# Kernel tuning notes

Measured on AMD Instinct MI355X. Metric: run time of the kernel, lower is better.

The kernel has to match this reference:

```python
import jax, jax.numpy as jnp
import numpy as np

N_NODES = 100000
N_EDGES = 1600000
IN_C, HID_C, OUT_C = 128, 128, 40


def setup_inputs() -> dict:
    key = jax.random.key(0)
    ks = jax.random.split(key, 10)
    def lin(k, fin, fout):
        return jax.random.normal(k, (fin, fout), jnp.float32) / np.sqrt(fin).astype(np.float32)
    return {
        "x": jax.random.normal(ks[0], (N_NODES, IN_C), jnp.float32),
        "edge_index": jax.random.randint(ks[1], (2, N_EDGES), 0, N_NODES, jnp.int64),
        "W1a": lin(ks[2], IN_C, HID_C), "b1a": jnp.zeros((HID_C,), jnp.float32),
        "W1b": lin(ks[3], HID_C, HID_C), "b1b": jnp.zeros((HID_C,), jnp.float32),
        "W2a": lin(ks[4], HID_C, HID_C), "b2a": jnp.zeros((HID_C,), jnp.float32),
        "W2b": lin(ks[5], HID_C, OUT_C), "b2b": jnp.zeros((OUT_C,), jnp.float32),
    }


def gin_conv(x, edge_index, Wa, ba, Wb, bb):
    # GINConv with eps=0: h_i = MLP(x_i + sum_{j in N(i)} x_j)
    src, dst = edge_index[0], edge_index[1]
    agg = jax.ops.segment_sum(x[src], dst, num_segments=N_NODES)  # [N, C]
    h = x + agg
    h = jnp.maximum(h @ Wa + ba, 0.0)  # Linear + ReLU
    return h @ Wb + bb                 # Linear


def reference(x, edge_index, W1a, b1a, W1b, b1b, W2a, b2a, W2b, b2b):
    h = gin_conv(x, edge_index, W1a, b1a, W1b, b1b)
    h = jnp.maximum(h, 0.0)
    # dropout(p=0.5) treated as identity (eval mode / deterministic reference)
    h = gin_conv(h, edge_index, W2a, b2a, W2b, b2b)
    return jax.nn.log_softmax(h, axis=1)
```

## Files before the change

kernel.cpp:

```cpp
#include <hip/hip_runtime.h>

#define N_NODES 100000
#define N_EDGES 1600000
#define CH 128
#define OUTC 40
#define CAP 64
#define NBKT 98
#define BKT_CAP 18432
#define P1_EDGES 4096
#define ROW4 16
#define QROW2 16
#define QSCALE (6.5f / 127.0f)
#define QINV   (127.0f / 6.5f)

typedef __attribute__((ext_vector_type(8))) short bf16x8s;
typedef __attribute__((ext_vector_type(4))) float f32x4;

__device__ __forceinline__ unsigned short f2b_rne(float f) {
    union { float f; unsigned int u; } c; c.f = f;
    unsigned int r = (c.u + 0x7FFF + ((c.u >> 16) & 1)) >> 16;
    return (unsigned short)r;
}
__device__ __forceinline__ float b2f(unsigned short b) {
    union { float f; unsigned int u; } c; c.u = ((unsigned int)b) << 16;
    return c.f;
}
__device__ __forceinline__ int q8(float f) {
    return __float2int_rn(fminf(fmaxf(f * QINV, -127.f), 127.f));
}
__device__ __forceinline__ void addq4(int* a, unsigned int v) {
    a[0] += (int)(v << 24) >> 24;
    a[1] += (int)(v << 16) >> 24;
    a[2] += (int)(v << 8) >> 24;
    a[3] += (int)v >> 24;
}

__global__ __launch_bounds__(256) void conv_f32_bf16_i8(const float4* __restrict__ in,
                                                        ushort4* __restrict__ outb,
                                                        uint2* __restrict__ outq, int n8) {
    int i = blockIdx.x * 256 + threadIdx.x;
    if (i >= n8) return;
    float4 a = in[i * 2], b = in[i * 2 + 1];
    ushort4 o0, o1;
    o0.x = f2b_rne(a.x); o0.y = f2b_rne(a.y); o0.z = f2b_rne(a.z); o0.w = f2b_rne(a.w);
    o1.x = f2b_rne(b.x); o1.y = f2b_rne(b.y); o1.z = f2b_rne(b.z); o1.w = f2b_rne(b.w);
    outb[i * 2] = o0; outb[i * 2 + 1] = o1;
    uint2 q;
    q.x = (unsigned)(q8(a.x) & 0xFF) | ((unsigned)(q8(a.y) & 0xFF) << 8) |
          ((unsigned)(q8(a.z) & 0xFF) << 16) | ((unsigned)(q8(a.w) & 0xFF) << 24);
    q.y = (unsigned)(q8(b.x) & 0xFF) | ((unsigned)(q8(b.y) & 0xFF) << 8) |
          ((unsigned)(q8(b.z) & 0xFF) << 16) | ((unsigned)(q8(b.w) & 0xFF) << 24);
    outq[i] = q;
}

__global__ __launch_bounds__(256) void zero_ints(int* __restrict__ p, int n) {
    int i = blockIdx.x * 256 + threadIdx.x;
    if (i < n) p[i] = 0;
}

__global__ __launch_bounds__(256) void bin_edges(const int* __restrict__ esrc,
                                                 const int* __restrict__ edst,
                                                 int* __restrict__ gcursor,
                                                 unsigned int* __restrict__ bins) {
    __shared__ uint2 stage[P1_EDGES];
    __shared__ int lcnt[NBKT];
    __shared__ int lofs[NBKT];
    __shared__ int lpos[NBKT];
    __shared__ int gbase[NBKT];
    const int tid = threadIdx.x;
    const int e0 = blockIdx.x * P1_EDGES;

    for (int i = tid; i < NBKT; i += 256) lcnt[i] = 0;
    __syncthreads();

    int s[16], d[16];
#pragma unroll
    for (int i = 0; i < 16; ++i) {
        int e = e0 + i * 256 + tid;
        if (e < N_EDGES) { s[i] = esrc[e]; d[i] = edst[e]; }
        else d[i] = -1;
    }
#pragma unroll
    for (int i = 0; i < 16; ++i)
        if (d[i] >= 0) atomicAdd(&lcnt[d[i] >> 10], 1);
    __syncthreads();

    if (tid < NBKT) lofs[tid] = lcnt[tid];
    __syncthreads();
    for (int dd = 1; dd < NBKT; dd <<= 1) {
        int v = 0;
        if (tid < NBKT && tid >= dd) v = lofs[tid - dd];
        __syncthreads();
        if (tid < NBKT) lofs[tid] += v;
        __syncthreads();
    }
    if (tid < NBKT) {
        lpos[tid] = lofs[tid] - lcnt[tid];
        gbase[tid] = atomicAdd(&gcursor[tid], lcnt[tid]);
    }
    __syncthreads();

#pragma unroll
    for (int i = 0; i < 16; ++i) {
        if (d[i] >= 0) {
            int b = d[i] >> 10;
            int slot = atomicAdd(&lpos[b], 1);
            stage[slot] = make_uint2((unsigned)s[i], (unsigned)d[i]);
        }
    }
    __syncthreads();

    int total = lofs[NBKT - 1];
    for (int r = tid; r < total; r += 256) {
        uint2 rec = stage[r];
        int b = (int)(rec.y >> 10);
        int excl = lofs[b] - lcnt[b];
        int pos = gbase[b] + (r - excl);
        unsigned p = ((rec.y & 1023u) << 17) | rec.x;
        if (pos < BKT_CAP) bins[(size_t)b * BKT_CAP + pos] = p;
    }
}

__global__ __launch_bounds__(256) void build_from_bins(const unsigned int* __restrict__ bins,
                                                       const int* __restrict__ gcursor,
                                                       int* __restrict__ adj,
                                                       int* __restrict__ cnt) {
    __shared__ int lc[1024];
    const int b = blockIdx.x;
    const int tid = threadIdx.x;
    const int base = b << 10;
    for (int i = tid; i < 1024; i += 256) lc[i] = 0;
    __syncthreads();
    int n = gcursor[b]; if (n > BKT_CAP) n = BKT_CAP;
    const unsigned int* myb = bins + (size_t)b * BKT_CAP;
    for (int i = tid; i < n; i += 256) {
        unsigned p = myb[i];
        int local = (int)(p >> 17);
        int src = (int)(p & 0x1FFFFu);
        int slot = atomicAdd(&lc[local], 1);
        if (slot < CAP) adj[((base + local) << 6) + slot] = src;
    }
    __syncthreads();
    for (int i = tid; i < 1024; i += 256) {
        int node = base + i;
        if (node < N_NODES) cnt[node] = lc[i];
    }
}

__global__ __launch_bounds__(256) void pack_w3(const float* __restrict__ W0,
                                               const float* __restrict__ W1,
                                               const float* __restrict__ W2,
                                               unsigned short* __restrict__ P0,
                                               unsigned short* __restrict__ P1,
                                               unsigned short* __restrict__ P2) {
    int t = blockIdx.x * 256 + threadIdx.x;
    if (t >= 3 * 2048) return;
    int which = t >> 11;
    int rem = t & 2047;
    int lane = rem & 63;
    int ks = (rem >> 6) & 3;
    int nt = rem >> 8;
    const float* W = which == 0 ? W0 : (which == 1 ? W1 : W2);
    unsigned short* P = which == 0 ? P0 : (which == 1 ? P1 : P2);
    int n = nt * 16 + (lane & 15);
    int kbase = ks * 32 + (lane >> 4) * 8;
    unsigned short* dst = P + ((nt * 4 + ks) * 64 + lane) * 8;
#pragma unroll
    for (int j = 0; j < 8; ++j)
        dst[j] = f2b_rne(W[(kbase + j) * CH + n]);
}

__global__ __launch_bounds__(256) void pack_wout(const float* __restrict__ W,
                                                 unsigned short* __restrict__ P) {
    int t = blockIdx.x * 256 + threadIdx.x;
    if (t >= 768) return;
    int nt = t >> 8, rem = t & 255;
    int ks = rem >> 6, lane = rem & 63;
    int n = nt * 16 + (lane & 15);
    int kbase = ks * 32 + (lane >> 4) * 8;
    unsigned short* dst = P + ((nt * 4 + ks) * 64 + lane) * 8;
#pragma unroll
    for (int j = 0; j < 8; ++j)
        dst[j] = (n < OUTC) ? f2b_rne(W[(kbase + j) * OUTC + n]) : (unsigned short)0;
}

template <bool FIXED>
__device__ __forceinline__ void gather_i8_body(const unsigned int* __restrict__ xq,
                                               const unsigned short* __restrict__ xb,
                                               const int* __restrict__ adj,
                                               const int* __restrict__ cnt,
                                               const unsigned int* __restrict__ hmax,
                                               unsigned short* __restrict__ agg) {
    int node = blockIdx.x * 4 + (threadIdx.x >> 6);
    int lane = threadIdx.x & 63;
    if (node >= N_NODES) return;
    int grp = lane >> 4, l16 = lane & 15;
    const uint2* q2 = reinterpret_cast<const uint2*>(xq);
    const uint4* f4 = reinterpret_cast<const uint4*>(xb);

    unsigned int nbu = (unsigned int)adj[(node << 6) + lane];
    int deg = cnt[node];
    uint4 sv = f4[node * ROW4 + l16];
    if (deg > CAP) deg = CAP;
    if (nbu > (unsigned)(N_NODES - 1)) nbu = N_NODES - 1;
    int nb = (int)nbu;

    float dq;
    if (FIXED) dq = QSCALE;
    else {
        union { unsigned u; float f; } c; c.u = hmax[0];
        dq = c.f * (1.0f / 127.0f);
    }

    int qa[8];
#pragma unroll
    for (int c = 0; c < 8; ++c) qa[c] = 0;

    const uint2 z2 = make_uint2(0, 0);
    for (int j = 0; j < deg; j += 16) {
        int j0 = j + grp, j1 = j0 + 4, j2 = j0 + 8, j3 = j0 + 12;
        int s0 = __shfl(nb, j0, 64);
        int s1 = __shfl(nb, j1, 64);
        int s2 = __shfl(nb, j2, 64);
        int s3 = __shfl(nb, j3, 64);
        uint2 v0 = (j0 < deg) ? q2[s0 * QROW2 + l16] : z2;
        uint2 v1 = (j1 < deg) ? q2[s1 * QROW2 + l16] : z2;
        uint2 v2 = (j2 < deg) ? q2[s2 * QROW2 + l16] : z2;
        uint2 v3 = (j3 < deg) ? q2[s3 * QROW2 + l16] : z2;
        addq4(qa, v0.x); addq4(qa + 4, v0.y);
        addq4(qa, v1.x); addq4(qa + 4, v1.y);
        addq4(qa, v2.x); addq4(qa + 4, v2.y);
        addq4(qa, v3.x); addq4(qa + 4, v3.y);
    }
#pragma unroll
    for (int c = 0; c < 8; ++c) {
        qa[c] += __shfl_xor(qa[c], 16, 64);
        qa[c] += __shfl_xor(qa[c], 32, 64);
    }
    if (grp == 0) {
        float a0 = b2f((unsigned short)(sv.x & 0xFFFF)) + dq * (float)qa[0];
        float a1 = b2f((unsigned short)(sv.x >> 16)) + dq * (float)qa[1];
        float a2 = b2f((unsigned short)(sv.y & 0xFFFF)) + dq * (float)qa[2];
        float a3 = b2f((unsigned short)(sv.y >> 16)) + dq * (float)qa[3];
        float a4 = b2f((unsigned short)(sv.z & 0xFFFF)) + dq * (float)qa[4];
        float a5 = b2f((unsigned short)(sv.z >> 16)) + dq * (float)qa[5];
        float a6 = b2f((unsigned short)(sv.w & 0xFFFF)) + dq * (float)qa[6];
        float a7 = b2f((unsigned short)(sv.w >> 16)) + dq * (float)qa[7];
        uint4 o;
        o.x = (unsigned)f2b_rne(a0) | ((unsigned)f2b_rne(a1) << 16);
        o.y = (unsigned)f2b_rne(a2) | ((unsigned)f2b_rne(a3) << 16);
        o.z = (unsigned)f2b_rne(a4) | ((unsigned)f2b_rne(a5) << 16);
        o.w = (unsigned)f2b_rne(a6) | ((unsigned)f2b_rne(a7) << 16);
        reinterpret_cast<uint4*>(agg)[node * ROW4 + l16] = o;
    }
}

__global__ __launch_bounds__(256) void gather_agg_i8(const unsigned int* __restrict__ xq,
                                                     const unsigned short* __restrict__ xb,
                                                     const int* __restrict__ adj,
                                                     const int* __restrict__ cnt,
                                                     unsigned short* __restrict__ agg) {
    gather_i8_body<true>(xq, xb, adj, cnt, nullptr, agg);
}

__global__ __launch_bounds__(256) void gather_agg_i8_dyn(const unsigned int* __restrict__ xq,
                                                         const unsigned short* __restrict__ xb,
                                                         const int* __restrict__ adj,
                                                         const int* __restrict__ cnt,
                                                         const unsigned int* __restrict__ hmax,
                                                         unsigned short* __restrict__ agg) {
    gather_i8_body<false>(xq, xb, adj, cnt, hmax, agg);
}

__global__ __launch_bounds__(256) void reduce_max(const float* __restrict__ bmax, int n,
                                                  unsigned int* __restrict__ hmax) {
    float m = 0.f;
    for (int i = threadIdx.x; i < n; i += 256) m = fmaxf(m, bmax[i]);
#pragma unroll
    for (int off = 1; off < 64; off <<= 1) m = fmaxf(m, __shfl_xor(m, off, 64));
    __shared__ float wm[4];
    if ((threadIdx.x & 63) == 0) wm[threadIdx.x >> 6] = m;
    __syncthreads();
    if (threadIdx.x == 0)
        hmax[0] = __float_as_uint(fmaxf(fmaxf(wm[0], wm[1]), fmaxf(wm[2], wm[3])));
}

__global__ __launch_bounds__(256) void quant_h1(const uint4* __restrict__ h1,
                                                const unsigned int* __restrict__ hmax,
                                                uint2* __restrict__ outq, int n8) {
    int i = blockIdx.x * 256 + threadIdx.x;
    if (i >= n8) return;
    union { unsigned u; float f; } c; c.u = hmax[0];
    float inv = 127.0f / fmaxf(c.f, 1e-30f);
    uint4 v = h1[i];
    int q[8];
    q[0] = __float2int_rn(fminf(b2f((unsigned short)(v.x & 0xFFFF)) * inv, 127.f));
    q[1] = __float2int_rn(fminf(b2f((unsigned short)(v.x >> 16)) * inv, 127.f));
    q[2] = __float2int_rn(fminf(b2f((unsigned short)(v.y & 0xFFFF)) * inv, 127.f));
    q[3] = __float2int_rn(fminf(b2f((unsigned short)(v.y >> 16)) * inv, 127.f));
    q[4] = __float2int_rn(fminf(b2f((unsigned short)(v.z & 0xFFFF)) * inv, 127.f));
    q[5] = __float2int_rn(fminf(b2f((unsigned short)(v.z >> 16)) * inv, 127.f));
    q[6] = __float2int_rn(fminf(b2f((unsigned short)(v.w & 0xFFFF)) * inv, 127.f));
    q[7] = __float2int_rn(fminf(b2f((unsigned short)(v.w >> 16)) * inv, 127.f));
    uint2 o;
    o.x = (unsigned)(q[0] & 0xFF) | ((unsigned)(q[1] & 0xFF) << 8) |
          ((unsigned)(q[2] & 0xFF) << 16) | ((unsigned)(q[3] & 0xFF) << 24);
    o.y = (unsigned)(q[4] & 0xFF) | ((unsigned)(q[5] & 0xFF) << 8) |
          ((unsigned)(q[6] & 0xFF) << 16) | ((unsigned)(q[7] & 0xFF) << 24);
    outq[i] = o;
}

__global__ __launch_bounds__(256) void gin_mlp_fused(const unsigned short* __restrict__ A,
                                                     const unsigned short* __restrict__ Pa,
                                                     const float* __restrict__ ba,
                                                     const unsigned short* __restrict__ Pb2,
                                                     const float* __restrict__ bb,
                                                     unsigned short* __restrict__ Cout,
                                                     float* __restrict__ bmax,
                                                     int M) {
    __shared__ unsigned short As[64 * 136];
    __shared__ float sm_max[4];
    const int row0 = blockIdx.x * 64;
    const int tid = threadIdx.x;
    const int wave = tid >> 6;
    const int lane = tid & 63;
    const int quad = lane >> 4;
    const int l15 = lane & 15;
    const int nt0 = wave * 2;

    bf16x8s b1f[2][4];
#pragma unroll
    for (int c = 0; c < 2; ++c)
#pragma unroll
        for (int ks = 0; ks < 4; ++ks)
            b1f[c][ks] = *reinterpret_cast<const bf16x8s*>(
                Pa + (((nt0 + c) * 4 + ks) * 64 + lane) * 8);

    {
        int r = tid & 63, seg = tid >> 6;
        int row = row0 + r;
        uint4 z = make_uint4(0, 0, 0, 0);
        const uint4* src = reinterpret_cast<const uint4*>(A + (long long)row * CH + seg * 32);
        uint4* dst = reinterpret_cast<uint4*>(&As[r * 136 + seg * 32]);
#pragma unroll
        for (int i = 0; i < 4; ++i)
            dst[i] = (row < M) ? src[i] : z;
    }
    __syncthreads();

    f32x4 acc[2][4];
#pragma unroll
    for (int c = 0; c < 2; ++c)
#pragma unroll
        for (int t = 0; t < 4; ++t) acc[c][t] = (f32x4){0.f, 0.f, 0.f, 0.f};
#pragma unroll
    for (int t = 0; t < 4; ++t)
#pragma unroll
        for (int ks = 0; ks < 4; ++ks) {
            bf16x8s af = *reinterpret_cast<const bf16x8s*>(
                &As[(t * 16 + l15) * 136 + ks * 32 + quad * 8]);
            acc[0][t] = __builtin_amdgcn_mfma_f32_16x16x32_bf16(af, b1f[0][ks], acc[0][t], 0, 0, 0);
            acc[1][t] = __builtin_amdgcn_mfma_f32_16x16x32_bf16(af, b1f[1][ks], acc[1][t], 0, 0, 0);
        }

    bf16x8s b2f[2][4];
#pragma unroll
    for (int c = 0; c < 2; ++c)
#pragma unroll
        for (int ks = 0; ks < 4; ++ks)
            b2f[c][ks] = *reinterpret_cast<const bf16x8s*>(
                Pb2 + (((nt0 + c) * 4 + ks) * 64 + lane) * 8);

    __syncthreads();
#pragma unroll
    for (int c = 0; c < 2; ++c) {
        int col = (nt0 + c) * 16 + l15;
        float bv = ba[col];
#pragma unroll
        for (int t = 0; t < 4; ++t)
#pragma unroll
            for (int r = 0; r < 4; ++r) {
                int rl = t * 16 + quad * 4 + r;
                As[rl * 136 + col] = f2b_rne(fmaxf(acc[c][t][r] + bv, 0.f));
            }
    }
    __syncthreads();

    f32x4 a2[2][4];
#pragma unroll
    for (int c = 0; c < 2; ++c)
#pragma unroll
        for (int t = 0; t < 4; ++t) a2[c][t] = (f32x4){0.f, 0.f, 0.f, 0.f};
#pragma unroll
    for (int t = 0; t < 4; ++t)
#pragma unroll
        for (int ks = 0; ks < 4; ++ks) {
            bf16x8s af = *reinterpret_cast<const bf16x8s*>(
                &As[(t * 16 + l15) * 136 + ks * 32 + quad * 8]);
            a2[0][t] = __builtin_amdgcn_mfma_f32_16x16x32_bf16(af, b2f[0][ks], a2[0][t], 0, 0, 0);
            a2[1][t] = __builtin_amdgcn_mfma_f32_16x16x32_bf16(af, b2f[1][ks], a2[1][t], 0, 0, 0);
        }
    __syncthreads();

    float wmax = 0.f;
#pragma unroll
    for (int c = 0; c < 2; ++c) {
        int col = (nt0 + c) * 16 + l15;
        float bv = bb[col];
#pragma unroll
        for (int t = 0; t < 4; ++t)
#pragma unroll
            for (int r = 0; r < 4; ++r) {
                int rl = t * 16 + quad * 4 + r;
                float v = fmaxf(a2[c][t][r] + bv, 0.f);
                if (row0 + rl < M) wmax = fmaxf(wmax, v);
                As[rl * 136 + col] = f2b_rne(v);
            }
    }
#pragma unroll
    for (int off = 1; off < 64; off <<= 1) wmax = fmaxf(wmax, __shfl_xor(wmax, off, 64));
    if (lane == 0) sm_max[wave] = wmax;
    __syncthreads();

    {
        int r = tid >> 2;
        int q = tid & 3;
        int row = row0 + r;
        if (row < M) {
            uint4* dst = reinterpret_cast<uint4*>(Cout + (long long)row * CH + q * 32);
            const unsigned short* sp = &As[r * 136 + q * 32];
#pragma unroll
            for (int i = 0; i < 4; ++i)
                dst[i] = *reinterpret_cast<const uint4*>(sp + i * 8);
        }
        if (tid == 0)
            bmax[blockIdx.x] = fmaxf(fmaxf(sm_max[0], sm_max[1]),
                                     fmaxf(sm_max[2], sm_max[3]));
    }
}

__global__ __launch_bounds__(256) void gin_out_fused(const unsigned short* __restrict__ A,
                                                     const unsigned short* __restrict__ Pa,
                                                     const float* __restrict__ ba,
                                                     const unsigned short* __restrict__ Pb,
                                                     const float* __restrict__ bias,
                                                     float* __restrict__ out, int M) {
    __shared__ unsigned short As[64 * 136];
    const int row0 = blockIdx.x * 64;
    const int tid = threadIdx.x;
    const int wave = tid >> 6;
    const int lane = tid & 63;
    const int quad = lane >> 4;
    const int l15 = lane & 15;
    const int nt0 = wave * 2;

    bf16x8s b1f[2][4];
#pragma unroll
    for (int c = 0; c < 2; ++c)
#pragma unroll
        for (int ks = 0; ks < 4; ++ks)
            b1f[c][ks] = *reinterpret_cast<const bf16x8s*>(
                Pa + (((nt0 + c) * 4 + ks) * 64 + lane) * 8);

    {
        int r = tid & 63, seg = tid >> 6;
        int row = row0 + r;
        uint4 z = make_uint4(0, 0, 0, 0);
        const uint4* src = reinterpret_cast<const uint4*>(A + (long long)row * CH + seg * 32);
        uint4* dst = reinterpret_cast<uint4*>(&As[r * 136 + seg * 32]);
#pragma unroll
        for (int i = 0; i < 4; ++i)
            dst[i] = (row < M) ? src[i] : z;
    }
    __syncthreads();

    f32x4 acc[2][4];
#pragma unroll
    for (int c = 0; c < 2; ++c)
#pragma unroll
        for (int t = 0; t < 4; ++t) acc[c][t] = (f32x4){0.f, 0.f, 0.f, 0.f};
#pragma unroll
    for (int t = 0; t < 4; ++t)
#pragma unroll
        for (int ks = 0; ks < 4; ++ks) {
            bf16x8s af = *reinterpret_cast<const bf16x8s*>(
                &As[(t * 16 + l15) * 136 + ks * 32 + quad * 8]);
            acc[0][t] = __builtin_amdgcn_mfma_f32_16x16x32_bf16(af, b1f[0][ks], acc[0][t], 0, 0, 0);
            acc[1][t] = __builtin_amdgcn_mfma_f32_16x16x32_bf16(af, b1f[1][ks], acc[1][t], 0, 0, 0);
        }

    bf16x8s bof[3][4];
#pragma unroll
    for (int nt = 0; nt < 3; ++nt)
#pragma unroll
        for (int ks = 0; ks < 4; ++ks)
            bof[nt][ks] = *reinterpret_cast<const bf16x8s*>(
                Pb + ((nt * 4 + ks) * 64 + lane) * 8);

    __syncthreads();
#pragma unroll
    for (int c = 0; c < 2; ++c) {
        int col = (nt0 + c) * 16 + l15;
        float bv = ba[col];
#pragma unroll
        for (int t = 0; t < 4; ++t)
#pragma unroll
            for (int r = 0; r < 4; ++r) {
                int rl = t * 16 + quad * 4 + r;
                As[rl * 136 + col] = f2b_rne(fmaxf(acc[c][t][r] + bv, 0.f));
            }
    }
    __syncthreads();

    f32x4 oacc[3];
#pragma unroll
    for (int nt = 0; nt < 3; ++nt) oacc[nt] = (f32x4){0.f, 0.f, 0.f, 0.f};
#pragma unroll
    for (int ks = 0; ks < 4; ++ks) {
        bf16x8s af = *reinterpret_cast<const bf16x8s*>(
            &As[(wave * 16 + l15) * 136 + ks * 32 + quad * 8]);
#pragma unroll
        for (int nt = 0; nt < 3; ++nt)
            oacc[nt] = __builtin_amdgcn_mfma_f32_16x16x32_bf16(af, bof[nt][ks], oacc[nt], 0, 0, 0);
    }

    const float b0v = bias[l15];
    const float b1v = bias[16 + l15];
    const float b2v = (l15 < 8) ? bias[32 + l15] : 0.f;
#pragma unroll
    for (int r = 0; r < 4; ++r) {
        int row = row0 + wave * 16 + quad * 4 + r;
        float v0 = oacc[0][r] + b0v;
        float v1 = oacc[1][r] + b1v;
        float v2 = (l15 < 8) ? (oacc[2][r] + b2v) : -1e30f;
        float m = fmaxf(fmaxf(v0, v1), v2);
#pragma unroll
        for (int off = 1; off < 16; off <<= 1) m = fmaxf(m, __shfl_xor(m, off, 64));
        float s = __expf(v0 - m) + __expf(v1 - m) + ((l15 < 8) ? __expf(v2 - m) : 0.f);
#pragma unroll
        for (int off = 1; off < 16; off <<= 1) s += __shfl_xor(s, off, 64);
        float lg = m + __logf(s);
        if (row < M) {
            float* orow = out + (long long)row * OUTC;
            orow[l15] = v0 - lg;
            orow[16 + l15] = v1 - lg;
            if (l15 < 8) orow[32 + l15] = v2 - lg;
        }
    }
}

extern "C" void kernel_launch(void* const* d_in, const int* in_sizes, int n_in,
                              void* d_out, int out_size, void* d_ws, size_t ws_size,
                              hipStream_t stream) {
    const float* x   = (const float*)d_in[0];
    const int* eidx  = (const int*)d_in[1];
    const int* esrc  = eidx;
    const int* edst  = eidx + N_EDGES;
    const float* W1a = (const float*)d_in[2];
    const float* b1a = (const float*)d_in[3];
    const float* W1b = (const float*)d_in[4];
    const float* b1b = (const float*)d_in[5];
    const float* W2a = (const float*)d_in[6];
    const float* b2a = (const float*)d_in[7];
    const float* W2b = (const float*)d_in[8];
    const float* b2b = (const float*)d_in[9];
    float* out = (float*)d_out;

    const size_t fe = (size_t)N_NODES * CH;
    unsigned short* xb  = (unsigned short*)d_ws;
    unsigned short* b0  = xb + fe;
    unsigned short* b1  = b0 + fe;
    unsigned int* xq    = (unsigned int*)(b1 + fe);
    unsigned int* h1q   = xq + fe / 4;
    int* adj     = (int*)(h1q + fe / 4);
    int* cnt     = adj + (size_t)N_NODES * CAP;
    int* gcursor = cnt + N_NODES;
    unsigned int* hmax = (unsigned int*)(gcursor + NBKT);
    float* bmax = (float*)(hmax + 2);
    unsigned int* bins = (unsigned int*)(bmax + 1568);
    unsigned short* P1 = (unsigned short*)(bins + (size_t)NBKT * BKT_CAP);
    unsigned short* P2 = P1 + 16384;
    unsigned short* P3 = P2 + 16384;
    unsigned short* Pb = P3 + 16384;

    const int conv_grid  = (int)((fe / 8 + 255) / 256);
    const int bin_grid   = (N_EDGES + P1_EDGES - 1) / P1_EDGES;
    const int gath_grid  = (N_NODES + 3) / 4;
    const int gemm_grid  = (N_NODES + 63) / 64;
    const int q8_grid    = (int)((fe / 8 + 255) / 256);

    conv_f32_bf16_i8<<<conv_grid, 256, 0, stream>>>((const float4*)x, (ushort4*)xb,
                                                    (uint2*)xq, (int)(fe / 8));
    zero_ints<<<1, 256, 0, stream>>>(gcursor, NBKT);
    bin_edges<<<bin_grid, 256, 0, stream>>>(esrc, edst, gcursor, bins);
    build_from_bins<<<NBKT, 256, 0, stream>>>(bins, gcursor, adj, cnt);
    pack_w3<<<24, 256, 0, stream>>>(W1a, W1b, W2a, P1, P2, P3);
    pack_wout<<<3, 256, 0, stream>>>(W2b, Pb);

    gather_agg_i8<<<gath_grid, 256, 0, stream>>>(xq, xb, adj, cnt, b0);
    gin_mlp_fused<<<gemm_grid, 256, 0, stream>>>(b0, P1, b1a, P2, b1b, b1, bmax, N_NODES);

    reduce_max<<<1, 256, 0, stream>>>(bmax, gemm_grid, hmax);
    quant_h1<<<q8_grid, 256, 0, stream>>>((const uint4*)b1, hmax, (uint2*)h1q, (int)(fe / 8));
    gather_agg_i8_dyn<<<gath_grid, 256, 0, stream>>>(h1q, b1, adj, cnt, hmax, b0);
    gin_out_fused<<<gemm_grid, 256, 0, stream>>>(b0, P3, b2a, Pb, b2b, out, N_NODES);
}
```

Baseline: 311.2 us.

## Use offset-binary uint8 features with packed perm accumulation and zero-row padding

Quantized features are now stored as unsigned offset-binary bytes (value+128), and the gather accumulates two bytes per 32-bit register using v_perm byte shuffles into 16-bit lanes. The per-element sign extension is replaced, and the bias is subtracted once at the end. Adjacency rows are padded up to a multiple of 16 with a dedicated zero row, so the inner loop no longer needs per-load degree predicates. This cuts ALU work in the gather loop at the cost of extra padding writes during graph build. Correctness relies on the 16-bit partial sums not overflowing.

```diff
diff --git a/kernel.cpp b/kernel.cpp
--- a/kernel.cpp
+++ b/kernel.cpp
@@ -12,6 +12,7 @@
 #define QROW2 16
 #define QSCALE (6.5f / 127.0f)
 #define QINV   (127.0f / 6.5f)
+#define ZROW N_NODES
 
 typedef __attribute__((ext_vector_type(8))) short bf16x8s;
 typedef __attribute__((ext_vector_type(4))) float f32x4;
@@ -27,12 +28,6 @@
 }
 __device__ __forceinline__ int q8(float f) {
     return __float2int_rn(fminf(fmaxf(f * QINV, -127.f), 127.f));
-}
-__device__ __forceinline__ void addq4(int* a, unsigned int v) {
-    a[0] += (int)(v << 24) >> 24;
-    a[1] += (int)(v << 16) >> 24;
-    a[2] += (int)(v << 8) >> 24;
-    a[3] += (int)v >> 24;
 }
 
 __global__ __launch_bounds__(256) void conv_f32_bf16_i8(const float4* __restrict__ in,
@@ -46,16 +41,23 @@
     o1.x = f2b_rne(b.x); o1.y = f2b_rne(b.y); o1.z = f2b_rne(b.z); o1.w = f2b_rne(b.w);
     outb[i * 2] = o0; outb[i * 2 + 1] = o1;
     uint2 q;
-    q.x = (unsigned)(q8(a.x) & 0xFF) | ((unsigned)(q8(a.y) & 0xFF) << 8) |
-          ((unsigned)(q8(a.z) & 0xFF) << 16) | ((unsigned)(q8(a.w) & 0xFF) << 24);
-    q.y = (unsigned)(q8(b.x) & 0xFF) | ((unsigned)(q8(b.y) & 0xFF) << 8) |
-          ((unsigned)(q8(b.z) & 0xFF) << 16) | ((unsigned)(q8(b.w) & 0xFF) << 24);
+    q.x = (unsigned)((q8(a.x) + 128) & 0xFF) | (((unsigned)((q8(a.y) + 128) & 0xFF)) << 8) |
+          (((unsigned)((q8(a.z) + 128) & 0xFF)) << 16) | (((unsigned)((q8(a.w) + 128) & 0xFF)) << 24);
+    q.y = (unsigned)((q8(b.x) + 128) & 0xFF) | (((unsigned)((q8(b.y) + 128) & 0xFF)) << 8) |
+          (((unsigned)((q8(b.z) + 128) & 0xFF)) << 16) | (((unsigned)((q8(b.w) + 128) & 0xFF)) << 24);
     outq[i] = q;
 }
 
-__global__ __launch_bounds__(256) void zero_ints(int* __restrict__ p, int n) {
-    int i = blockIdx.x * 256 + threadIdx.x;
-    if (i < n) p[i] = 0;
+__global__ __launch_bounds__(256) void setup_misc(int* __restrict__ gcursor,
+                                                  unsigned int* __restrict__ xq,
+                                                  unsigned int* __restrict__ h1q) {
+    int t = threadIdx.x;
+    if (t < NBKT) gcursor[t] = 0;
+    if (t >= 128 && t < 160) {
+        int i = t - 128;
+        xq[(size_t)ZROW * 32 + i] = 0x80808080u;
+        h1q[(size_t)ZROW * 32 + i] = 0x80808080u;
+    }
 }
 
 __global__ __launch_bounds__(256) void bin_edges(const int* __restrict__ esrc,
@@ -143,7 +145,14 @@
     __syncthreads();
     for (int i = tid; i < 1024; i += 256) {
         int node = base + i;
-        if (node < N_NODES) cnt[node] = lc[i];
+        if (node < N_NODES) {
+            int dg = lc[i];
+            cnt[node] = dg;
+            int s0 = dg > CAP ? CAP : dg;
+            int nr = (s0 + 15) & ~15;
+            for (int s = s0; s < nr; ++s)
+                adj[(node << 6) + s] = ZROW;
+        }
     }
 }
 
@@ -185,7 +194,7 @@
 }
 
 template <bool FIXED>
-__device__ __forceinline__ void gather_i8_body(const unsigned int* __restrict__ xq,
+__device__ __forceinline__ void gather_u8_body(const unsigned int* __restrict__ xq,
                                                const unsigned short* __restrict__ xb,
                                                const int* __restrict__ adj,
                                                const int* __restrict__ cnt,
@@ -198,12 +207,11 @@
     const uint2* q2 = reinterpret_cast<const uint2*>(xq);
     const uint4* f4 = reinterpret_cast<const uint4*>(xb);
 
-    unsigned int nbu = (unsigned int)adj[(node << 6) + lane];
     int deg = cnt[node];
+    if (deg > CAP) deg = CAP;
+    int nr = (deg + 15) & ~15;
+    int nb = (lane < nr) ? adj[(node << 6) + lane] : 0;
     uint4 sv = f4[node * ROW4 + l16];
-    if (deg > CAP) deg = CAP;
-    if (nbu > (unsigned)(N_NODES - 1)) nbu = N_NODES - 1;
-    int nb = (int)nbu;
 
     float dq;
     if (FIXED) dq = QSCALE;
@@ -212,64 +220,82 @@
         dq = c.f * (1.0f / 127.0f);
     }
 
-    int qa[8];
-#pragma unroll
-    for (int c = 0; c < 8; ++c) qa[c] = 0;
-
-    const uint2 z2 = make_uint2(0, 0);
-    for (int j = 0; j < deg; j += 16) {
-        int j0 = j + grp, j1 = j0 + 4, j2 = j0 + 8, j3 = j0 + 12;
+    unsigned a0 = 0, a1 = 0, a2 = 0, a3 = 0;
+
+    for (int j = 0; j < nr; j += 16) {
+        int j0 = j + grp;
         int s0 = __shfl(nb, j0, 64);
-        int s1 = __shfl(nb, j1, 64);
-        int s2 = __shfl(nb, j2, 64);
-        int s3 = __shfl(nb, j3, 64);
-        uint2 v0 = (j0 < deg) ? q2[s0 * QROW2 + l16] : z2;
-        uint2 v1 = (j1 < deg) ? q2[s1 * QROW2 + l16] : z2;
-        uint2 v2 = (j2 < deg) ? q2[s2 * QROW2 + l16] : z2;
-        uint2 v3 = (j3 < deg) ? q2[s3 * QROW2 + l16] : z2;
-        addq4(qa, v0.x); addq4(qa + 4, v0.y);
-        addq4(qa, v1.x); addq4(qa + 4, v1.y);
-        addq4(qa, v2.x); addq4(qa + 4, v2.y);
-        addq4(qa, v3.x); addq4(qa + 4, v3.y);
-    }
-#pragma unroll
-    for (int c = 0; c < 8; ++c) {
-        qa[c] += __shfl_xor(qa[c], 16, 64);
-        qa[c] += __shfl_xor(qa[c], 32, 64);
-    }
+        int s1 = __shfl(nb, j0 + 4, 64);
+        int s2 = __shfl(nb, j0 + 8, 64);
+        int s3 = __shfl(nb, j0 + 12, 64);
+        uint2 v0 = q2[s0 * QROW2 + l16];
+        uint2 v1 = q2[s1 * QROW2 + l16];
+        uint2 v2 = q2[s2 * QROW2 + l16];
+        uint2 v3 = q2[s3 * QROW2 + l16];
+        a0 += __builtin_amdgcn_perm(v0.x, v0.x, 0x0C020C00u);
+        a1 += __builtin_amdgcn_perm(v0.x, v0.x, 0x0C030C01u);
+        a2 += __builtin_amdgcn_perm(v0.y, v0.y, 0x0C020C00u);
+        a3 += __builtin_amdgcn_perm(v0.y, v0.y, 0x0C030C01u);
+        a0 += __builtin_amdgcn_perm(v1.x, v1.x, 0x0C020C00u);
+        a1 += __builtin_amdgcn_perm(v1.x, v1.x, 0x0C030C01u);
+        a2 += __builtin_amdgcn_perm(v1.y, v1.y, 0x0C020C00u);
+        a3 += __builtin_amdgcn_perm(v1.y, v1.y, 0x0C030C01u);
+        a0 += __builtin_amdgcn_perm(v2.x, v2.x, 0x0C020C00u);
+        a1 += __builtin_amdgcn_perm(v2.x, v2.x, 0x0C030C01u);
+        a2 += __builtin_amdgcn_perm(v2.y, v2.y, 0x0C020C00u);
+        a3 += __builtin_amdgcn_perm(v2.y, v2.y, 0x0C030C01u);
+        a0 += __builtin_amdgcn_perm(v3.x, v3.x, 0x0C020C00u);
+        a1 += __builtin_amdgcn_perm(v3.x, v3.x, 0x0C030C01u);
+        a2 += __builtin_amdgcn_perm(v3.y, v3.y, 0x0C020C00u);
+        a3 += __builtin_amdgcn_perm(v3.y, v3.y, 0x0C030C01u);
+    }
+    a0 += (unsigned)__shfl_xor((int)a0, 16, 64); a0 += (unsigned)__shfl_xor((int)a0, 32, 64);
+    a1 += (unsigned)__shfl_xor((int)a1, 16, 64); a1 += (unsigned)__shfl_xor((int)a1, 32, 64);
+    a2 += (unsigned)__shfl_xor((int)a2, 16, 64); a2 += (unsigned)__shfl_xor((int)a2, 32, 64);
+    a3 += (unsigned)__shfl_xor((int)a3, 16, 64); a3 += (unsigned)__shfl_xor((int)a3, 32, 64);
+
     if (grp == 0) {
-        float a0 = b2f((unsigned short)(sv.x & 0xFFFF)) + dq * (float)qa[0];
-        float a1 = b2f((unsigned short)(sv.x >> 16)) + dq * (float)qa[1];
-        float a2 = b2f((unsigned short)(sv.y & 0xFFFF)) + dq * (float)qa[2];
-        float a3 = b2f((unsigned short)(sv.y >> 16)) + dq * (float)qa[3];
-        float a4 = b2f((unsigned short)(sv.z & 0xFFFF)) + dq * (float)qa[4];
-        float a5 = b2f((unsigned short)(sv.z >> 16)) + dq * (float)qa[5];
-        float a6 = b2f((unsigned short)(sv.w & 0xFFFF)) + dq * (float)qa[6];
-        float a7 = b2f((unsigned short)(sv.w >> 16)) + dq * (float)qa[7];
+        int bias = nr << 7;
+        float q0 = (float)((int)(a0 & 0xFFFFu) - bias);
+        float q1 = (float)((int)(a1 & 0xFFFFu) - bias);
+        float q2c = (float)((int)(a0 >> 16) - bias);
+        float q3 = (float)((int)(a1 >> 16) - bias);
+        float q4 = (float)((int)(a2 & 0xFFFFu) - bias);
+        float q5 = (float)((int)(a3 & 0xFFFFu) - bias);
+        float q6 = (float)((int)(a2 >> 16) - bias);
+        float q7 = (float)((int)(a3 >> 16) - bias);
+        float r0 = b2f((unsigned short)(sv.x & 0xFFFF)) + dq * q0;
+        float r1 = b2f((unsigned short)(sv.x >> 16)) + dq * q1;
+        float r2 = b2f((unsigned short)(sv.y & 0xFFFF)) + dq * q2c;
+        float r3 = b2f((unsigned short)(sv.y >> 16)) + dq * q3;
+        float r4 = b2f((unsigned short)(sv.z & 0xFFFF)) + dq * q4;
+        float r5 = b2f((unsigned short)(sv.z >> 16)) + dq * q5;
+        float r6 = b2f((unsigned short)(sv.w & 0xFFFF)) + dq * q6;
+        float r7 = b2f((unsigned short)(sv.w >> 16)) + dq * q7;
         uint4 o;
-        o.x = (unsigned)f2b_rne(a0) | ((unsigned)f2b_rne(a1) << 16);
-        o.y = (unsigned)f2b_rne(a2) | ((unsigned)f2b_rne(a3) << 16);
-        o.z = (unsigned)f2b_rne(a4) | ((unsigned)f2b_rne(a5) << 16);
-        o.w = (unsigned)f2b_rne(a6) | ((unsigned)f2b_rne(a7) << 16);
+        o.x = (unsigned)f2b_rne(r0) | ((unsigned)f2b_rne(r1) << 16);
+        o.y = (unsigned)f2b_rne(r2) | ((unsigned)f2b_rne(r3) << 16);
+        o.z = (unsigned)f2b_rne(r4) | ((unsigned)f2b_rne(r5) << 16);
+        o.w = (unsigned)f2b_rne(r6) | ((unsigned)f2b_rne(r7) << 16);
         reinterpret_cast<uint4*>(agg)[node * ROW4 + l16] = o;
     }
 }
 
-__global__ __launch_bounds__(256) void gather_agg_i8(const unsigned int* __restrict__ xq,
+__global__ __launch_bounds__(256) void gather_agg_u8(const unsigned int* __restrict__ xq,
                                                      const unsigned short* __restrict__ xb,
                                                      const int* __restrict__ adj,
                                                      const int* __restrict__ cnt,
                                                      unsigned short* __restrict__ agg) {
-    gather_i8_body<true>(xq, xb, adj, cnt, nullptr, agg);
-}
-
-__global__ __launch_bounds__(256) void gather_agg_i8_dyn(const unsigned int* __restrict__ xq,
+    gather_u8_body<true>(xq, xb, adj, cnt, nullptr, agg);
+}
+
+__global__ __launch_bounds__(256) void gather_agg_u8_dyn(const unsigned int* __restrict__ xq,
                                                          const unsigned short* __restrict__ xb,
                                                          const int* __restrict__ adj,
                                                          const int* __restrict__ cnt,
                                                          const unsigned int* __restrict__ hmax,
                                                          unsigned short* __restrict__ agg) {
-    gather_i8_body<false>(xq, xb, adj, cnt, hmax, agg);
+    gather_u8_body<false>(xq, xb, adj, cnt, hmax, agg);
 }
 
 __global__ __launch_bounds__(256) void reduce_max(const float* __restrict__ bmax, int n,
@@ -303,10 +329,10 @@
     q[6] = __float2int_rn(fminf(b2f((unsigned short)(v.w & 0xFFFF)) * inv, 127.f));
     q[7] = __float2int_rn(fminf(b2f((unsigned short)(v.w >> 16)) * inv, 127.f));
     uint2 o;
-    o.x = (unsigned)(q[0] & 0xFF) | ((unsigned)(q[1] & 0xFF) << 8) |
-          ((unsigned)(q[2] & 0xFF) << 16) | ((unsigned)(q[3] & 0xFF) << 24);
-    o.y = (unsigned)(q[4] & 0xFF) | ((unsigned)(q[5] & 0xFF) << 8) |
-          ((unsigned)(q[6] & 0xFF) << 16) | ((unsigned)(q[7] & 0xFF) << 24);
+    o.x = (unsigned)((q[0] + 128) & 0xFF) | (((unsigned)((q[1] + 128) & 0xFF)) << 8) |
+          (((unsigned)((q[2] + 128) & 0xFF)) << 16) | (((unsigned)((q[3] + 128) & 0xFF)) << 24);
+    o.y = (unsigned)((q[4] + 128) & 0xFF) | (((unsigned)((q[5] + 128) & 0xFF)) << 8) |
+          (((unsigned)((q[6] + 128) & 0xFF)) << 16) | (((unsigned)((q[7] + 128) & 0xFF)) << 24);
     outq[i] = o;
 }
 
@@ -363,12 +389,12 @@
             acc[1][t] = __builtin_amdgcn_mfma_f32_16x16x32_bf16(af, b1f[1][ks], acc[1][t], 0, 0, 0);
         }
 
-    bf16x8s b2f[2][4];
+    bf16x8s b2f_[2][4];
 #pragma unroll
     for (int c = 0; c < 2; ++c)
 #pragma unroll
         for (int ks = 0; ks < 4; ++ks)
-            b2f[c][ks] = *reinterpret_cast<const bf16x8s*>(
+            b2f_[c][ks] = *reinterpret_cast<const bf16x8s*>(
                 Pb2 + (((nt0 + c) * 4 + ks) * 64 + lane) * 8);
 
     __syncthreads();
@@ -397,8 +423,8 @@
         for (int ks = 0; ks < 4; ++ks) {
             bf16x8s af = *reinterpret_cast<const bf16x8s*>(
                 &As[(t * 16 + l15) * 136 + ks * 32 + quad * 8]);
-            a2[0][t] = __builtin_amdgcn_mfma_f32_16x16x32_bf16(af, b2f[0][ks], a2[0][t], 0, 0, 0);
-            a2[1][t] = __builtin_amdgcn_mfma_f32_16x16x32_bf16(af, b2f[1][ks], a2[1][t], 0, 0, 0);
+            a2[0][t] = __builtin_amdgcn_mfma_f32_16x16x32_bf16(af, b2f_[0][ks], a2[0][t], 0, 0, 0);
+            a2[1][t] = __builtin_amdgcn_mfma_f32_16x16x32_bf16(af, b2f_[1][ks], a2[1][t], 0, 0, 0);
         }
     __syncthreads();
 
@@ -567,12 +593,13 @@
     float* out = (float*)d_out;
 
     const size_t fe = (size_t)N_NODES * CH;
+    const size_t qrow_pad = 32;
     unsigned short* xb  = (unsigned short*)d_ws;
     unsigned short* b0  = xb + fe;
     unsigned short* b1  = b0 + fe;
     unsigned int* xq    = (unsigned int*)(b1 + fe);
-    unsigned int* h1q   = xq + fe / 4;
-    int* adj     = (int*)(h1q + fe / 4);
+    unsigned int* h1q   = xq + fe / 4 + qrow_pad;
+    int* adj     = (int*)(h1q + fe / 4 + qrow_pad);
     int* cnt     = adj + (size_t)N_NODES * CAP;
     int* gcursor = cnt + N_NODES;
     unsigned int* hmax = (unsigned int*)(gcursor + NBKT);
@@ -591,17 +618,17 @@
 
     conv_f32_bf16_i8<<<conv_grid, 256, 0, stream>>>((const float4*)x, (ushort4*)xb,
                                                     (uint2*)xq, (int)(fe / 8));
-    zero_ints<<<1, 256, 0, stream>>>(gcursor, NBKT);
+    setup_misc<<<1, 256, 0, stream>>>(gcursor, xq, h1q);
     bin_edges<<<bin_grid, 256, 0, stream>>>(esrc, edst, gcursor, bins);
     build_from_bins<<<NBKT, 256, 0, stream>>>(bins, gcursor, adj, cnt);
     pack_w3<<<24, 256, 0, stream>>>(W1a, W1b, W2a, P1, P2, P3);
     pack_wout<<<3, 256, 0, stream>>>(W2b, Pb);
 
-    gather_agg_i8<<<gath_grid, 256, 0, stream>>>(xq, xb, adj, cnt, b0);
+    gather_agg_u8<<<gath_grid, 256, 0, stream>>>(xq, xb, adj, cnt, b0);
     gin_mlp_fused<<<gemm_grid, 256, 0, stream>>>(b0, P1, b1a, P2, b1b, b1, bmax, N_NODES);
 
     reduce_max<<<1, 256, 0, stream>>>(bmax, gemm_grid, hmax);
     quant_h1<<<q8_grid, 256, 0, stream>>>((const uint4*)b1, hmax, (uint2*)h1q, (int)(fe / 8));
-    gather_agg_i8_dyn<<<gath_grid, 256, 0, stream>>>(h1q, b1, adj, cnt, hmax, b0);
+    gather_agg_u8_dyn<<<gath_grid, 256, 0, stream>>>(h1q, b1, adj, cnt, hmax, b0);
     gin_out_fused<<<gemm_grid, 256, 0, stream>>>(b0, P3, b2a, Pb, b2b, out, N_NODES);
 }
```

New measurement: 299.9 us. 3.6% less time.
